# Optimization experiments

Hardware: AMD Instinct MI355X
Metric: run time of the kernel (lower is better)

## Reference

```python
import jax, jax.numpy as jnp
import numpy as np

DIM = 1024
NUM_HEADS = 16
HEAD_DIM = DIM // NUM_HEADS


def setup_inputs() -> dict:
    key = jax.random.key(0)
    k1, k2, k3, k4, k5, k6 = jax.random.split(key, 6)
    B, T, C = 4, 2048, DIM
    s = 1.0 / np.sqrt(C)
    return {
        "x": jax.random.normal(k1, (B, T, C), dtype=jnp.float32),
        "attn_bias": jax.random.normal(k2, (B, T, T), dtype=jnp.float32),
        "qkv_w": jax.random.uniform(k3, (3 * C, C), dtype=jnp.float32, minval=-s, maxval=s),
        "qkv_b": jax.random.uniform(k4, (3 * C,), dtype=jnp.float32, minval=-s, maxval=s),
        "out_w": jax.random.uniform(k5, (C, C), dtype=jnp.float32, minval=-s, maxval=s),
        "out_b": jax.random.uniform(k6, (C,), dtype=jnp.float32, minval=-s, maxval=s),
    }


def reference(x, attn_bias, qkv_w, qkv_b, out_w, out_b):
    B, T, C = x.shape
    H, D = NUM_HEADS, HEAD_DIM
    # fused QKV projection (torch Linear: x @ W^T + b)
    qkv = jnp.einsum('btc,fc->btf', x, qkv_w) + qkv_b  # [B,T,3C]
    q, k, v = jnp.split(qkv, 3, axis=-1)
    q = q.reshape(B, T, H, D).transpose(0, 2, 1, 3)  # [B,H,T,D]
    k = k.reshape(B, T, H, D).transpose(0, 2, 1, 3)
    v = v.reshape(B, T, H, D).transpose(0, 2, 1, 3)
    scores = jnp.einsum('bhtd,bhsd->bhts', q, k) / jnp.sqrt(jnp.float32(D))
    scores = scores + attn_bias[:, None, :, :]  # 3-D bias -> broadcast over heads
    attn = jax.nn.softmax(scores, axis=-1)
    out = jnp.einsum('bhts,bhsd->bhtd', attn, v)  # [B,H,T,D]
    out = out.transpose(0, 2, 1, 3).reshape(B, T, C)
    return jnp.einsum('btc,fc->btf', out, out_w) + out_b
```

## Files before the change

### kernel.cpp

```cpp
#include <hip/hip_runtime.h>

#define BATCH 4
#define SEQ   2048
#define CDIM  1024
#define HEADS 16
#define HDIM  64
#define N3    3072
#define NTOK  8192
#define QKP   2048
#define LOG2E 1.44269504f
#define QSC   0.18033688f

typedef __attribute__((ext_vector_type(4))) float    float4v;
typedef __attribute__((ext_vector_type(8))) short    short8;
typedef __attribute__((ext_vector_type(8))) __bf16   bf16x8;
typedef __attribute__((ext_vector_type(4))) _Float16 half4v;
typedef __attribute__((ext_vector_type(2))) _Float16 half2v;

__device__ __forceinline__ unsigned short f2bf(float f) {
    union { float f; unsigned int u; } x; x.f = f;
    unsigned int r = x.u + 0x7fffu + ((x.u >> 16) & 1u);
    return (unsigned short)(r >> 16);
}

__device__ __forceinline__ bf16x8 ld_bf8(const unsigned short* p) {
    short8 s = *(const short8*)p;
    return __builtin_bit_cast(bf16x8, s);
}

__device__ __forceinline__ void glds16(const void* g, void* l) {
    __builtin_amdgcn_global_load_lds(
        (const __attribute__((address_space(1))) void*)g,
        (__attribute__((address_space(3))) void*)l, 16, 0, 0);
}

__global__ void cast_f32_bf16(const float* __restrict__ in,
                              unsigned short* __restrict__ out, int n4) {
    int i = blockIdx.x * blockDim.x + threadIdx.x;
    if (i >= n4) return;
    float4v v = ((const float4v*)in)[i];
    ushort4 r;
    r.x = f2bf(v[0]); r.y = f2bf(v[1]); r.z = f2bf(v[2]); r.w = f2bf(v[3]);
    ((ushort4*)out)[i] = r;
}

__global__ __launch_bounds__(256, 3)
void gemm_bt(const unsigned short* __restrict__ A,
             const unsigned short* __restrict__ Bm,
             const float* __restrict__ bias,
             void* __restrict__ Cout,
             void* __restrict__ Cout2,
             int M, int N, int K, int mode)
{
    __shared__ alignas(16) unsigned short As[128 * 64];
    __shared__ alignas(16) unsigned short Bs[128 * 64];

    const int tid  = threadIdx.x;
    const int lane = tid & 63;
    const int wave = tid >> 6;
    const int wr = wave >> 1, wc = wave & 1;
    const int lm = lane & 15, quad = lane >> 4;

    const int nwg  = gridDim.x * gridDim.y;
    const int d    = blockIdx.y * gridDim.x + blockIdx.x;
    const int orig = (d & 7) * (nwg >> 3) + (d >> 3);
    const int bix  = orig % gridDim.x;
    const int biy  = orig / gridDim.x;

    const size_t m0 = (size_t)biy * 128;
    const size_t n0 = (size_t)bix * 128;

    const unsigned short* ag[4];
    const unsigned short* bg[4];
    unsigned short* la[4];
    unsigned short* lb[4];
#pragma unroll
    for (int i = 0; i < 4; i++) {
        int idx = tid + i * 256;
        int row = idx >> 3;
        int lc  = (idx & 7) ^ (row & 7);
        ag[i] = &A [(m0 + row) * K + lc * 8];
        bg[i] = &Bm[(n0 + row) * K + lc * 8];
        la[i] = &As[(idx & ~63) * 8];
        lb[i] = &Bs[(idx & ~63) * 8];
    }

    float4v acc[4][4];
#pragma unroll
    for (int i = 0; i < 4; i++)
#pragma unroll
        for (int j = 0; j < 4; j++) acc[i][j] = (float4v){0.f, 0.f, 0.f, 0.f};

    for (int k0 = 0; k0 < K; k0 += 64) {
#pragma unroll
        for (int i = 0; i < 4; i++) glds16(ag[i], la[i]);
#pragma unroll
        for (int i = 0; i < 4; i++) glds16(bg[i], lb[i]);
#pragma unroll
        for (int i = 0; i < 4; i++) { ag[i] += 64; bg[i] += 64; }
        __syncthreads();
#pragma unroll
        for (int kk = 0; kk < 2; kk++) {
            bf16x8 af[4], bfr[4];
#pragma unroll
            for (int t = 0; t < 4; t++) {
                int slot = ((quad + kk * 4) ^ (lm & 7)) * 8;
                af [t] = ld_bf8(&As[(wr * 64 + t * 16 + lm) * 64 + slot]);
                bfr[t] = ld_bf8(&Bs[(wc * 64 + t * 16 + lm) * 64 + slot]);
            }
#pragma unroll
            for (int ti = 0; ti < 4; ti++)
#pragma unroll
                for (int tj = 0; tj < 4; tj++)
                    acc[ti][tj] = __builtin_amdgcn_mfma_f32_16x16x32_bf16(
                        af[ti], bfr[tj], acc[ti][tj], 0, 0, 0);
        }
        __syncthreads();
    }

#pragma unroll
    for (int ti = 0; ti < 4; ti++) {
        size_t row = m0 + wr * 64 + ti * 16 + quad * 4;
#pragma unroll
        for (int tj = 0; tj < 4; tj++) {
            int col = (int)n0 + wc * 64 + tj * 16 + lm;
            float bv = bias[col];
            if (mode == 0) {
#pragma unroll
                for (int r = 0; r < 4; r++)
                    ((float*)Cout)[(row + r) * N + col] = acc[ti][tj][r] + bv;
            } else if (col < 2 * CDIM) {
                float scl = (col < CDIM) ? QSC : 1.0f;
#pragma unroll
                for (int r = 0; r < 4; r++)
                    ((unsigned short*)Cout)[(row + r) * QKP + col] =
                        f2bf((acc[ti][tj][r] + bv) * scl);
            } else {
                int hd = col - 2 * CDIM;
                int bb = (int)(row >> 11);
                int s  = (int)(row & 2047);
                half4v hv;
#pragma unroll
                for (int r = 0; r < 4; r++) hv[r] = (_Float16)(acc[ti][tj][r] + bv);
                *(half4v*)((unsigned short*)Cout2 +
                           ((size_t)bb * CDIM + hd) * SEQ + s) = hv;
            }
        }
    }
}

__global__ __launch_bounds__(512, 6)
void attn_kernel(const unsigned short* __restrict__ qk,
                 const unsigned short* __restrict__ vT,
                 const float* __restrict__ bias,
                 unsigned short* __restrict__ outp)
{
    __shared__ alignas(16) unsigned short Ks [64 * 64];
    __shared__ alignas(16) unsigned short Vts[64 * 64];
    __shared__ alignas(16) float          BiasS[128 * 64];

    const int tid  = threadIdx.x;
    const int lane = tid & 63, wave = tid >> 6;
    const int lm = lane & 15, quad = lane >> 4;
    const int q0 = blockIdx.x * 128;
    const int bh = blockIdx.y;
    const int bb = bh >> 4, h = bh & 15;
    const size_t rowbase = (size_t)bb * SEQ;
    const unsigned short* vTh = vT + (size_t)bh * HDIM * SEQ;
    const float* biasb = bias + (size_t)bb * SEQ * SEQ + (size_t)q0 * SEQ;

    bf16x8 bq[2];
    {
        const unsigned short* qrow =
            &qk[(rowbase + q0 + wave * 16 + lm) * QKP + h * 64];
        bq[0] = ld_bf8(qrow + (quad    ) * 8);
        bq[1] = ld_bf8(qrow + (quad + 4) * 8);
    }

    const unsigned short *kg0, *vg0;
    unsigned short *lk0, *lv0;
    {
        int idx = tid, row = idx >> 3, lc = (idx & 7) ^ (row & 7);
        kg0 = &qk[(rowbase + row) * QKP + CDIM + h * 64 + lc * 8];
        vg0 = &vTh[(size_t)row * SEQ + lc * 8];
        lk0 = &Ks [(idx & ~63) * 8];
        lv0 = &Vts[(idx & ~63) * 8];
    }
    const float* bgp[4];
    float*       lbp[4];
#pragma unroll
    for (int i = 0; i < 4; i++) {
        int idx = tid + i * 512;
        int row = idx >> 4;
        int lc  = (idx & 15) ^ (row & 15);
        bgp[i] = &biasb[(size_t)row * SEQ + lc * 4];
        lbp[i] = &BiasS[(idx & ~63) * 4];
    }

    const half4v vones = {(_Float16)1.f, (_Float16)1.f, (_Float16)1.f, (_Float16)1.f};
    float4v rs4 = (float4v){0.f, 0.f, 0.f, 0.f};
    float4v o[4];
#pragma unroll
    for (int t = 0; t < 4; t++) o[t] = (float4v){0.f, 0.f, 0.f, 0.f};

    for (int it = 0; it < SEQ / 64; ++it) {
        __syncthreads();
        glds16(kg0, lk0);
        glds16(vg0, lv0);
#pragma unroll
        for (int i = 0; i < 4; i++) glds16(bgp[i], lbp[i]);
        kg0 += 64 * QKP;
        vg0 += 64;
#pragma unroll
        for (int i = 0; i < 4; i++) bgp[i] += 64;
        __syncthreads();

        float4v st[4];
#pragma unroll
        for (int tj = 0; tj < 4; ++tj) {
            float4v bv = *(const float4v*)&BiasS[(wave * 16 + lm) * 64 +
                                                 (((tj * 4 + quad) ^ lm) * 4)];
            st[tj] = bv * LOG2E;
            bf16x8 ak0 = ld_bf8(&Ks[(tj * 16 + lm) * 64 + (((quad    ) ^ (lm & 7)) * 8)]);
            bf16x8 ak1 = ld_bf8(&Ks[(tj * 16 + lm) * 64 + (((quad + 4) ^ (lm & 7)) * 8)]);
            st[tj] = __builtin_amdgcn_mfma_f32_16x16x32_bf16(ak0, bq[0], st[tj], 0, 0, 0);
            st[tj] = __builtin_amdgcn_mfma_f32_16x16x32_bf16(ak1, bq[1], st[tj], 0, 0, 0);
        }

        half4v pa[4];
#pragma unroll
        for (int tj = 0; tj < 4; ++tj) {
            float p0 = __builtin_amdgcn_exp2f(st[tj][0]);
            float p1 = __builtin_amdgcn_exp2f(st[tj][1]);
            float p2 = __builtin_amdgcn_exp2f(st[tj][2]);
            float p3 = __builtin_amdgcn_exp2f(st[tj][3]);
            half2v plo = __builtin_bit_cast(half2v, __builtin_amdgcn_cvt_pkrtz(p0, p1));
            half2v phi = __builtin_bit_cast(half2v, __builtin_amdgcn_cvt_pkrtz(p2, p3));
            pa[tj][0] = plo[0]; pa[tj][1] = plo[1];
            pa[tj][2] = phi[0]; pa[tj][3] = phi[1];
        }

#pragma unroll
        for (int tj = 0; tj < 4; ++tj)
            rs4 = __builtin_amdgcn_mfma_f32_16x16x16f16(pa[tj], vones, rs4, 0, 0, 0);

        __builtin_amdgcn_s_setprio(1);
#pragma unroll
        for (int tj = 0; tj < 4; ++tj) {
            int c = tj * 4 + quad;
#pragma unroll
            for (int dt = 0; dt < 4; ++dt) {
                int row = dt * 16 + lm;
                int off = (((c >> 1) ^ (lm & 7)) * 8) + (c & 1) * 4;
                half4v vb = *(const half4v*)&Vts[row * 64 + off];
                o[dt] = __builtin_amdgcn_mfma_f32_16x16x16f16(pa[tj], vb, o[dt], 0, 0, 0);
            }
        }
        __builtin_amdgcn_s_setprio(0);
    }

    float i4[4];
#pragma unroll
    for (int r = 0; r < 4; r++) i4[r] = 1.0f / rs4[r];
#pragma unroll
    for (int dt = 0; dt < 4; dt++) {
        int col = h * 64 + dt * 16 + lm;
#pragma unroll
        for (int r = 0; r < 4; r++) {
            size_t trow = rowbase + q0 + wave * 16 + quad * 4 + r;
            outp[trow * CDIM + col] = f2bf(o[dt][r] * i4[r]);
        }
    }
}

extern "C" void kernel_launch(void* const* d_in, const int* in_sizes, int n_in,
                              void* d_out, int out_size, void* d_ws, size_t ws_size,
                              hipStream_t stream)
{
    const float* x         = (const float*)d_in[0];
    const float* attn_bias = (const float*)d_in[1];
    const float* qkv_w     = (const float*)d_in[2];
    const float* qkv_b     = (const float*)d_in[3];
    const float* out_w     = (const float*)d_in[4];
    const float* out_b     = (const float*)d_in[5];
    float* out = (float*)d_out;

    char* p = (char*)d_ws;
    unsigned short* x_bf   = (unsigned short*)p; p += (size_t)NTOK * CDIM * 2;
    unsigned short* wq_bf  = (unsigned short*)p; p += (size_t)N3 * CDIM * 2;
    unsigned short* wo_bf  = (unsigned short*)p; p += (size_t)CDIM * CDIM * 2;
    unsigned short* qk_bf  = (unsigned short*)p; p += (size_t)NTOK * QKP * 2;
    unsigned short* vT_f16 = (unsigned short*)p; p += (size_t)BATCH * CDIM * SEQ * 2;
    unsigned short* at_bf  = (unsigned short*)p;

    int n4;
    n4 = NTOK * CDIM / 4;
    cast_f32_bf16<<<(n4 + 255) / 256, 256, 0, stream>>>(x, x_bf, n4);
    n4 = N3 * CDIM / 4;
    cast_f32_bf16<<<(n4 + 255) / 256, 256, 0, stream>>>(qkv_w, wq_bf, n4);
    n4 = CDIM * CDIM / 4;
    cast_f32_bf16<<<(n4 + 255) / 256, 256, 0, stream>>>(out_w, wo_bf, n4);

    gemm_bt<<<dim3(N3 / 128, NTOK / 128), 256, 0, stream>>>(
        x_bf, wq_bf, qkv_b, qk_bf, vT_f16, NTOK, N3, CDIM, 1);

    attn_kernel<<<dim3(SEQ / 128, BATCH * HEADS), 512, 0, stream>>>(
        qk_bf, vT_f16, attn_bias, at_bf);

    gemm_bt<<<dim3(CDIM / 128, NTOK / 128), 256, 0, stream>>>(
        at_bf, wo_bf, out_b, out, nullptr, NTOK, CDIM, CDIM, 0);
}
```

Measured before the change: 374.1 us.

## Prefetch K/V/bias tiles through registers and halve attention block size

The attention kernel drops the direct global-to-LDS async copies. It now loads the next K, V^T and bias tiles into registers during the current tile's compute, then writes them to shared memory at the start of the next iteration. The block shrinks from 512 to 256 threads with 64 query rows per block, which doubles the grid and halves the bias LDS buffer. This is meant to hide global load latency behind the MFMA and softmax work. The cost is extra register pressure from the prefetch buffers, and each block's K/V tile now serves only 64 query rows instead of 128, so K/V reuse drops.

After: 350.2 us. -6.4%, faster.

```diff
diff --git a/kernel.cpp b/kernel.cpp
--- a/kernel.cpp
+++ b/kernel.cpp
@@ -149,20 +149,20 @@
     }
 }
 
-__global__ __launch_bounds__(512, 6)
+__global__ __launch_bounds__(256, 4)
 void attn_kernel(const unsigned short* __restrict__ qk,
                  const unsigned short* __restrict__ vT,
                  const float* __restrict__ bias,
                  unsigned short* __restrict__ outp)
 {
-    __shared__ alignas(16) unsigned short Ks [64 * 64];
-    __shared__ alignas(16) unsigned short Vts[64 * 64];
-    __shared__ alignas(16) float          BiasS[128 * 64];
+    __shared__ alignas(16) unsigned short Ks  [64 * 64];
+    __shared__ alignas(16) unsigned short Vts [64 * 64];
+    __shared__ alignas(16) float          BiasS[64 * 64];
 
     const int tid  = threadIdx.x;
     const int lane = tid & 63, wave = tid >> 6;
     const int lm = lane & 15, quad = lane >> 4;
-    const int q0 = blockIdx.x * 128;
+    const int q0 = blockIdx.x * 64;
     const int bh = blockIdx.y;
     const int bb = bh >> 4, h = bh & 15;
     const size_t rowbase = (size_t)bb * SEQ;
@@ -177,25 +177,45 @@
         bq[1] = ld_bf8(qrow + (quad + 4) * 8);
     }
 
-    const unsigned short *kg0, *vg0;
-    unsigned short *lk0, *lv0;
+    const unsigned short *kg0, *kg1, *vg0, *vg1;
     {
         int idx = tid, row = idx >> 3, lc = (idx & 7) ^ (row & 7);
         kg0 = &qk[(rowbase + row) * QKP + CDIM + h * 64 + lc * 8];
         vg0 = &vTh[(size_t)row * SEQ + lc * 8];
-        lk0 = &Ks [(idx & ~63) * 8];
-        lv0 = &Vts[(idx & ~63) * 8];
-    }
-    const float* bgp[4];
-    float*       lbp[4];
-#pragma unroll
-    for (int i = 0; i < 4; i++) {
-        int idx = tid + i * 512;
-        int row = idx >> 4;
-        int lc  = (idx & 15) ^ (row & 15);
-        bgp[i] = &biasb[(size_t)row * SEQ + lc * 4];
-        lbp[i] = &BiasS[(idx & ~63) * 4];
-    }
+        idx = tid + 256; row = idx >> 3; lc = (idx & 7) ^ (row & 7);
+        kg1 = &qk[(rowbase + row) * QKP + CDIM + h * 64 + lc * 8];
+        vg1 = &vTh[(size_t)row * SEQ + lc * 8];
+    }
+    const float* bgp0; const float* bgp1; const float* bgp2; const float* bgp3;
+    {
+        int idx, row, lc;
+        idx = tid;       row = idx >> 4; lc = (idx & 15) ^ (row & 15);
+        bgp0 = &biasb[(size_t)row * SEQ + lc * 4];
+        idx = tid + 256; row = idx >> 4; lc = (idx & 15) ^ (row & 15);
+        bgp1 = &biasb[(size_t)row * SEQ + lc * 4];
+        idx = tid + 512; row = idx >> 4; lc = (idx & 15) ^ (row & 15);
+        bgp2 = &biasb[(size_t)row * SEQ + lc * 4];
+        idx = tid + 768; row = idx >> 4; lc = (idx & 15) ^ (row & 15);
+        bgp3 = &biasb[(size_t)row * SEQ + lc * 4];
+    }
+
+    unsigned short* lkd0 = &Ks [(size_t)tid * 8];
+    unsigned short* lkd1 = &Ks [((size_t)tid + 256) * 8];
+    unsigned short* lvd0 = &Vts[(size_t)tid * 8];
+    unsigned short* lvd1 = &Vts[((size_t)tid + 256) * 8];
+    float* lbd0 = &BiasS[(size_t)tid * 4];
+    float* lbd1 = &BiasS[((size_t)tid + 256) * 4];
+    float* lbd2 = &BiasS[((size_t)tid + 512) * 4];
+    float* lbd3 = &BiasS[((size_t)tid + 768) * 4];
+
+    short8  rk0 = *(const short8*)kg0;
+    short8  rk1 = *(const short8*)kg1;
+    short8  rv0 = *(const short8*)vg0;
+    short8  rv1 = *(const short8*)vg1;
+    float4v rb0 = *(const float4v*)bgp0;
+    float4v rb1 = *(const float4v*)bgp1;
+    float4v rb2 = *(const float4v*)bgp2;
+    float4v rb3 = *(const float4v*)bgp3;
 
     const half4v vones = {(_Float16)1.f, (_Float16)1.f, (_Float16)1.f, (_Float16)1.f};
     float4v rs4 = (float4v){0.f, 0.f, 0.f, 0.f};
@@ -205,15 +225,24 @@
 
     for (int it = 0; it < SEQ / 64; ++it) {
         __syncthreads();
-        glds16(kg0, lk0);
-        glds16(vg0, lv0);
-#pragma unroll
-        for (int i = 0; i < 4; i++) glds16(bgp[i], lbp[i]);
-        kg0 += 64 * QKP;
-        vg0 += 64;
-#pragma unroll
-        for (int i = 0; i < 4; i++) bgp[i] += 64;
+        *(short8*) lkd0 = rk0;  *(short8*) lkd1 = rk1;
+        *(short8*) lvd0 = rv0;  *(short8*) lvd1 = rv1;
+        *(float4v*)lbd0 = rb0;  *(float4v*)lbd1 = rb1;
+        *(float4v*)lbd2 = rb2;  *(float4v*)lbd3 = rb3;
         __syncthreads();
+
+        if (it < SEQ / 64 - 1) {
+            kg0 += 64 * QKP; kg1 += 64 * QKP; vg0 += 64; vg1 += 64;
+            bgp0 += 64; bgp1 += 64; bgp2 += 64; bgp3 += 64;
+            rk0 = *(const short8*)kg0;
+            rk1 = *(const short8*)kg1;
+            rv0 = *(const short8*)vg0;
+            rv1 = *(const short8*)vg1;
+            rb0 = *(const float4v*)bgp0;
+            rb1 = *(const float4v*)bgp1;
+            rb2 = *(const float4v*)bgp2;
+            rb3 = *(const float4v*)bgp3;
+        }
 
         float4v st[4];
 #pragma unroll
@@ -304,7 +333,7 @@
     gemm_bt<<<dim3(N3 / 128, NTOK / 128), 256, 0, stream>>>(
         x_bf, wq_bf, qkv_b, qk_bf, vT_f16, NTOK, N3, CDIM, 1);
 
-    attn_kernel<<<dim3(SEQ / 128, BATCH * HEADS), 512, 0, stream>>>(
+    attn_kernel<<<dim3(SEQ / 64, BATCH * HEADS), 256, 0, stream>>>(
         qk_bf, vT_f16, attn_bias, at_bf);
 
     gemm_bt<<<dim3(CDIM / 128, NTOK / 128), 256, 0, stream>>>(
```
